# Kernel optimization log

Hardware: AMD Instinct MI355X
Metric: run time of the kernel (lower is better)

Reference implementation:

```python
import jax, jax.numpy as jnp
import numpy as np


def setup_inputs() -> dict:
    key = jax.random.key(0)
    k1, k2, k3, k4 = jax.random.split(key, 4)
    B, D, H, A, T = 1024, 512, 512, 18, 64
    xs = jax.random.normal(k1, (B, D), dtype=jnp.float32)
    task_id = jax.random.randint(k2, (B,), 0, T, dtype=jnp.int64)
    # weight_init ~ scaled randn; biases start at zero per the module
    fc1_weights = jax.random.normal(k3, (T, D, H), dtype=jnp.float32) * (1.0 / np.sqrt(D))
    fc1_biases = jnp.zeros((T, H), dtype=jnp.float32)
    fc2_weights = jax.random.normal(k4, (T, H, A), dtype=jnp.float32) * (1.0 / np.sqrt(H))
    fc2_biases = jnp.zeros((T, A), dtype=jnp.float32)
    return {"xs": xs, "task_id": task_id, "fc1_weights": fc1_weights,
            "fc1_biases": fc1_biases, "fc2_weights": fc2_weights, "fc2_biases": fc2_biases}


def reference(xs, task_id, fc1_weights, fc1_biases, fc2_weights, fc2_biases):
    # per-sample task-indexed weight gather (as in the torch module)
    w1 = fc1_weights[task_id]            # [B, D, H]
    b1 = fc1_biases[task_id]             # [B, H]
    w2 = fc2_weights[task_id]            # [B, H, A]
    b2 = fc2_biases[task_id]             # [B, A]
    h = jax.nn.relu(jnp.einsum('bd,bdh->bh', xs, w1) + b1)   # batch_linear + relu
    logits = jnp.einsum('bh,bha->ba', h, w2) + b2             # batch_linear
    logp = jax.nn.log_softmax(logits, axis=-1)                # [B, A]
    # Categorical sample (fixed key for reproducibility)
    action = jax.random.categorical(jax.random.key(1), logits, axis=-1)  # [B]
    log_prob = jnp.take_along_axis(logp, action[:, None], axis=1)        # [B, 1]
    entropy = -jnp.sum(jnp.exp(logp) * logp, axis=1, keepdims=True)      # [B, 1]
    return action, log_prob, entropy
```

## Files before the change

### kernel.cpp

```cpp
#include <hip/hip_runtime.h>
#include <stdint.h>

#define B_N   1024
#define D_DIM 512
#define H_DIM 512
#define A_DIM 18
#define T_N   64
#define HTILE 256
#define SMAX  32

__device__ __forceinline__ bool taskid_is_int32(const int* raw, int lane) {
    int probe = raw[lane];
    unsigned long long odd = __ballot((lane & 1) && probe != 0);
    return odd != 0ull;
}

template <int KSP>
__global__ __launch_bounds__(256) void fc1_kernel(const float* __restrict__ xs,
                                                  const float* __restrict__ w1,
                                                  const int* __restrict__ raw,
                                                  float* __restrict__ hpre) {
    constexpr int DK = D_DIM / KSP;
    int task  = blockIdx.x;
    int htile = blockIdx.y;
    int ksp   = blockIdx.z;
    int lane = threadIdx.x & 63;
    int wv4  = threadIdx.x >> 6;

    __shared__ int slist[B_N];
    __shared__ int s_n;
    __shared__ __align__(16) float xlds[SMAX * DK];

    if (threadIdx.x < 64) {
        bool is32 = taskid_is_int32(raw, lane);
        int base = 0;
        for (int c = 0; c < B_N; c += 64) {
            int id = is32 ? raw[c + lane] : raw[2 * (c + lane)];
            unsigned long long m = __ballot(id == task);
            if (id == task) {
                unsigned long long below = m & ((1ull << lane) - 1ull);
                slist[base + __popcll(below)] = c + lane;
            }
            base += __popcll(m);
        }
        if (lane == 0) s_n = base;
    }
    __syncthreads();
    int n = s_n;
    if (n == 0) return;

    int hbase = htile * HTILE + lane * 4;
    int d0    = ksp * DK;
    const float* wbase = w1 + ((size_t)task * D_DIM + d0) * H_DIM + hbase;
    float* hout = hpre + (size_t)ksp * ((size_t)B_N * H_DIM);

    for (int sb = 0; sb < n; sb += SMAX) {
        int ns = min(SMAX, n - sb);
        for (int idx = threadIdx.x; idx < ns * DK; idx += 256) {
            int sl = idx / DK;
            int dl = idx - sl * DK;
            int smp = slist[sb + sl];
            xlds[idx] = xs[(size_t)smp * D_DIM + d0 + dl];
        }
        __syncthreads();

        float4 acc[8];
#pragma unroll
        for (int j = 0; j < 8; ++j) acc[j] = make_float4(0.f, 0.f, 0.f, 0.f);

        for (int d = 0; d < DK; d += 8) {
            float4 wvr[8];
#pragma unroll
            for (int u = 0; u < 8; ++u)
                wvr[u] = *(const float4*)(wbase + (size_t)(d + u) * H_DIM);
#pragma unroll
            for (int j = 0; j < 8; ++j) {
                int sl = wv4 + 4 * j;
                if (sl < ns) {
                    const float* xp = &xlds[sl * DK + d];
                    float4 xa = *(const float4*)xp;
                    float4 xb = *(const float4*)(xp + 4);
                    float xv[8] = {xa.x, xa.y, xa.z, xa.w, xb.x, xb.y, xb.z, xb.w};
#pragma unroll
                    for (int u = 0; u < 8; ++u) {
                        acc[j].x = fmaf(xv[u], wvr[u].x, acc[j].x);
                        acc[j].y = fmaf(xv[u], wvr[u].y, acc[j].y);
                        acc[j].z = fmaf(xv[u], wvr[u].z, acc[j].z);
                        acc[j].w = fmaf(xv[u], wvr[u].w, acc[j].w);
                    }
                }
            }
        }

#pragma unroll
        for (int j = 0; j < 8; ++j) {
            int sl = wv4 + 4 * j;
            if (sl < ns) {
                int smp = slist[sb + sl];
                *(float4*)(hout + (size_t)smp * H_DIM + hbase) = acc[j];
            }
        }
        __syncthreads();
    }
}

__device__ __forceinline__ uint32_t rotl32(uint32_t x, int r) {
    return (x << r) | (x >> (32 - r));
}

__device__ __forceinline__ uint32_t threefry_bits_part(uint32_t i) {
    uint32_t x0 = 0u;
    uint32_t x1 = i;
    const uint32_t ks0 = 0u, ks1 = 1u, ks2 = 0x1BD11BDAu ^ 0u ^ 1u;
    x0 += ks0; x1 += ks1;
#define TFR(r) { x0 += x1; x1 = rotl32(x1, (r)); x1 ^= x0; }
    TFR(13) TFR(15) TFR(26) TFR(6)
    x0 += ks1; x1 += ks2 + 1u;
    TFR(17) TFR(29) TFR(16) TFR(24)
    x0 += ks2; x1 += ks0 + 2u;
    TFR(13) TFR(15) TFR(26) TFR(6)
    x0 += ks0; x1 += ks1 + 3u;
    TFR(17) TFR(29) TFR(16) TFR(24)
    x0 += ks1; x1 += ks2 + 4u;
    TFR(13) TFR(15) TFR(26) TFR(6)
    x0 += ks2; x1 += ks0 + 5u;
#undef TFR
    return x0 ^ x1;
}

template <int KSP>
__global__ __launch_bounds__(64) void head_kernel(const int* __restrict__ raw,
                                                  const float* __restrict__ hpre,
                                                  const float* __restrict__ b1,
                                                  const float* __restrict__ w2,
                                                  const float* __restrict__ b2,
                                                  float* __restrict__ out) {
    __shared__ __align__(16) float w2l[H_DIM * A_DIM];
    __shared__ float red[16][A_DIM];
    __shared__ float logits_lds[A_DIM];

    int s = blockIdx.x;
    int lane = threadIdx.x;
    bool is32 = taskid_is_int32(raw, lane);
    int t = is32 ? raw[s] : raw[2 * s];

    const float4* g4 = (const float4*)(w2 + (size_t)t * (H_DIM * A_DIM));
    float4* l4 = (float4*)w2l;
#pragma unroll
    for (int i = 0; i < (H_DIM * A_DIM) / (64 * 4); ++i)
        l4[i * 64 + lane] = g4[i * 64 + lane];

    float hreg[H_DIM / 64];
#pragma unroll
    for (int k = 0; k < H_DIM / 64; ++k) {
        int h = lane + 64 * k;
        size_t p = (size_t)s * H_DIM + h;
        float v = b1[(size_t)t * H_DIM + h];
#pragma unroll
        for (int q = 0; q < KSP; ++q)
            v += hpre[(size_t)q * ((size_t)B_N * H_DIM) + p];
        hreg[k] = fmaxf(v, 0.f);
    }
    __syncthreads();

    float la[A_DIM];
#pragma unroll
    for (int a = 0; a < A_DIM; ++a) la[a] = 0.f;
#pragma unroll
    for (int k = 0; k < H_DIM / 64; ++k) {
        int h = lane + 64 * k;
        const float2* row = (const float2*)&w2l[h * A_DIM];
        float hk = hreg[k];
#pragma unroll
        for (int a2 = 0; a2 < A_DIM / 2; ++a2) {
            float2 ww = row[a2];
            la[2 * a2]     = fmaf(hk, ww.x, la[2 * a2]);
            la[2 * a2 + 1] = fmaf(hk, ww.y, la[2 * a2 + 1]);
        }
    }

#pragma unroll
    for (int a = 0; a < A_DIM; ++a) {
        la[a] += __shfl_xor(la[a], 1);
        la[a] += __shfl_xor(la[a], 2);
    }
    if ((lane & 3) == 0) {
        int g = lane >> 2;
#pragma unroll
        for (int a = 0; a < A_DIM; ++a) red[g][a] = la[a];
    }
    __syncthreads();
    if (lane < A_DIM) {
        float sum = b2[(size_t)t * A_DIM + lane];
#pragma unroll
        for (int g = 0; g < 16; ++g) sum += red[g][lane];
        logits_lds[lane] = sum;
    }
    __syncthreads();

    float lg = (lane < A_DIM) ? logits_lds[lane] : -INFINITY;

    float z = -INFINITY;
    if (lane < A_DIM) {
        uint32_t bits = threefry_bits_part((uint32_t)(s * A_DIM + lane));
        float f = __uint_as_float(0x3f800000u | (bits >> 9)) - 1.0f;
        float u = fmaxf(f, 1.17549435e-38f);
        float g = -logf(-logf(u));
        z = lg + g;
    }
    int idx = lane;
#pragma unroll
    for (int o = 1; o < 64; o <<= 1) {
        float oz = __shfl_xor(z, o);
        int   oi = __shfl_xor(idx, o);
        if (oz > z || (oz == z && oi < idx)) { z = oz; idx = oi; }
    }

    float mx = lg;
#pragma unroll
    for (int o = 1; o < 64; o <<= 1) mx = fmaxf(mx, __shfl_xor(mx, o));
    float e = (lane < A_DIM) ? expf(lg - mx) : 0.f;
#pragma unroll
    for (int o = 1; o < 64; o <<= 1) e += __shfl_xor(e, o);
    float lse = mx + logf(e);
    float lp = lg - lse;
    float c = (lane < A_DIM) ? expf(lp) * lp : 0.f;
#pragma unroll
    for (int o = 1; o < 64; o <<= 1) c += __shfl_xor(c, o);

    if (lane == 0) {
        out[s]             = (float)idx;
        out[B_N + s]       = logits_lds[idx] - lse;
        out[2 * B_N + s]   = -c;
    }
}

extern "C" void kernel_launch(void* const* d_in, const int* in_sizes, int n_in,
                              void* d_out, int out_size, void* d_ws, size_t ws_size,
                              hipStream_t stream) {
    const float* xs      = (const float*)d_in[0];
    const int*   traw    = (const int*)d_in[1];
    const float* w1      = (const float*)d_in[2];
    const float* b1      = (const float*)d_in[3];
    const float* w2      = (const float*)d_in[4];
    const float* b2      = (const float*)d_in[5];
    float* out = (float*)d_out;
    char*  ws  = (char*)d_ws;

    const size_t part_bytes = (size_t)B_N * H_DIM * sizeof(float);

    int ksp = 4;
    if (ws_size < 4 * part_bytes) ksp = 2;
    if (ws_size < 2 * part_bytes) ksp = 1;

    float* hpre = (float*)ws;

    if (ksp == 4) {
        fc1_kernel<4><<<dim3(T_N, 2, 4), 256, 0, stream>>>(xs, w1, traw, hpre);
        head_kernel<4><<<B_N, 64, 0, stream>>>(traw, hpre, b1, w2, b2, out);
    } else if (ksp == 2) {
        fc1_kernel<2><<<dim3(T_N, 2, 2), 256, 0, stream>>>(xs, w1, traw, hpre);
        head_kernel<2><<<B_N, 64, 0, stream>>>(traw, hpre, b1, w2, b2, out);
    } else {
        fc1_kernel<1><<<dim3(T_N, 2, 1), 256, 0, stream>>>(xs, w1, traw, hpre);
        head_kernel<1><<<B_N, 64, 0, stream>>>(traw, hpre, b1, w2, b2, out);
    }
}
```

Baseline: 133.1 us.

## Restructure fc1 to one column per thread with double-buffered weight loads

The fc1 kernel now gives each thread one H column and keeps accumulators for up to 32 samples in registers. Previously each thread covered four columns for a strided subset of samples. Weights are loaded as scalar columns in chunks of 16 rows and double-buffered, so the next chunk's loads overlap the FMAs of the current chunk. Every weight element is now reused across all samples in the thread instead of being reloaded by each of the four waves. The costs are higher register pressure (32 accumulators plus 32 weight registers), a broadcast LDS read pattern for x, and padding samples up to a multiple of 8. The xlds indexing assumes DK/4 == 32, which holds only for KSP=4.

```diff
diff --git a/kernel.cpp b/kernel.cpp
--- a/kernel.cpp
+++ b/kernel.cpp
@@ -21,17 +21,18 @@
                                                   const int* __restrict__ raw,
                                                   float* __restrict__ hpre) {
     constexpr int DK = D_DIM / KSP;
+    constexpr int NCHUNK = DK / 16;
     int task  = blockIdx.x;
     int htile = blockIdx.y;
     int ksp   = blockIdx.z;
-    int lane = threadIdx.x & 63;
-    int wv4  = threadIdx.x >> 6;
+    int tid   = threadIdx.x;
+    int lane  = tid & 63;
 
     __shared__ int slist[B_N];
     __shared__ int s_n;
-    __shared__ __align__(16) float xlds[SMAX * DK];
-
-    if (threadIdx.x < 64) {
+    __shared__ __align__(16) float xlds[SMAX][DK];
+
+    if (tid < 64) {
         bool is32 = taskid_is_int32(raw, lane);
         int base = 0;
         for (int c = 0; c < B_N; c += 64) {
@@ -49,55 +50,81 @@
     int n = s_n;
     if (n == 0) return;
 
-    int hbase = htile * HTILE + lane * 4;
-    int d0    = ksp * DK;
-    const float* wbase = w1 + ((size_t)task * D_DIM + d0) * H_DIM + hbase;
-    float* hout = hpre + (size_t)ksp * ((size_t)B_N * H_DIM);
+    int col = htile * HTILE + tid;
+    int d0  = ksp * DK;
+    const float* wcol = w1 + ((size_t)task * D_DIM + d0) * H_DIM + col;
+    float* hout = hpre + (size_t)ksp * ((size_t)B_N * H_DIM) + col;
 
     for (int sb = 0; sb < n; sb += SMAX) {
-        int ns = min(SMAX, n - sb);
-        for (int idx = threadIdx.x; idx < ns * DK; idx += 256) {
-            int sl = idx / DK;
-            int dl = idx - sl * DK;
-            int smp = slist[sb + sl];
-            xlds[idx] = xs[(size_t)smp * D_DIM + d0 + dl];
-        }
-        __syncthreads();
-
-        float4 acc[8];
-#pragma unroll
-        for (int j = 0; j < 8; ++j) acc[j] = make_float4(0.f, 0.f, 0.f, 0.f);
-
-        for (int d = 0; d < DK; d += 8) {
-            float4 wvr[8];
-#pragma unroll
-            for (int u = 0; u < 8; ++u)
-                wvr[u] = *(const float4*)(wbase + (size_t)(d + u) * H_DIM);
-#pragma unroll
-            for (int j = 0; j < 8; ++j) {
-                int sl = wv4 + 4 * j;
-                if (sl < ns) {
-                    const float* xp = &xlds[sl * DK + d];
-                    float4 xa = *(const float4*)xp;
-                    float4 xb = *(const float4*)(xp + 4);
-                    float xv[8] = {xa.x, xa.y, xa.z, xa.w, xb.x, xb.y, xb.z, xb.w};
-#pragma unroll
-                    for (int u = 0; u < 8; ++u) {
-                        acc[j].x = fmaf(xv[u], wvr[u].x, acc[j].x);
-                        acc[j].y = fmaf(xv[u], wvr[u].y, acc[j].y);
-                        acc[j].z = fmaf(xv[u], wvr[u].z, acc[j].z);
-                        acc[j].w = fmaf(xv[u], wvr[u].w, acc[j].w);
-                    }
-                }
-            }
-        }
-
-#pragma unroll
-        for (int j = 0; j < 8; ++j) {
-            int sl = wv4 + 4 * j;
+        int ns  = min(SMAX, n - sb);
+        int nsr = (ns + 7) & ~7;
+
+        for (int idx = tid; idx < nsr * (DK / 4); idx += 256) {
+            int sl = idx >> 5;
+            int f  = idx & (DK / 4 - 1);
+            float4 v = make_float4(0.f, 0.f, 0.f, 0.f);
             if (sl < ns) {
                 int smp = slist[sb + sl];
-                *(float4*)(hout + (size_t)smp * H_DIM + hbase) = acc[j];
+                v = *(const float4*)(xs + (size_t)smp * D_DIM + d0 + 4 * f);
+            }
+            *(float4*)(&xlds[sl][4 * f]) = v;
+        }
+        __syncthreads();
+
+        float acc[SMAX];
+#pragma unroll
+        for (int j = 0; j < SMAX; ++j) acc[j] = 0.f;
+
+        float wa[16], wb[16];
+
+#define LOADW(buf, cc)                                                        \
+        _Pragma("unroll")                                                     \
+        for (int u = 0; u < 16; ++u)                                          \
+            buf[u] = wcol[(size_t)((cc) * 16 + u) * H_DIM];
+
+#define COMPW(buf, cc) do {                                                   \
+        int dbase = (cc) * 16;                                                \
+        _Pragma("unroll")                                                     \
+        for (int jb = 0; jb < SMAX / 8; ++jb) {                               \
+            if (jb * 8 < nsr) {                                               \
+                _Pragma("unroll")                                             \
+                for (int jj = 0; jj < 8; ++jj) {                              \
+                    int j = jb * 8 + jj;                                      \
+                    float4 x0 = *(const float4*)(&xlds[j][dbase]);            \
+                    float4 x1 = *(const float4*)(&xlds[j][dbase + 4]);        \
+                    float4 x2 = *(const float4*)(&xlds[j][dbase + 8]);        \
+                    float4 x3 = *(const float4*)(&xlds[j][dbase + 12]);       \
+                    float xv[16] = {x0.x, x0.y, x0.z, x0.w,                   \
+                                    x1.x, x1.y, x1.z, x1.w,                   \
+                                    x2.x, x2.y, x2.z, x2.w,                   \
+                                    x3.x, x3.y, x3.z, x3.w};                  \
+                    _Pragma("unroll")                                         \
+                    for (int u = 0; u < 16; ++u)                              \
+                        acc[j] = fmaf(xv[u], buf[u], acc[j]);                 \
+                }                                                             \
+            }                                                                 \
+        }                                                                     \
+    } while (0)
+
+        LOADW(wa, 0);
+#pragma unroll
+        for (int c = 0; c < NCHUNK; ++c) {
+            if ((c & 1) == 0) {
+                if (c + 1 < NCHUNK) { LOADW(wb, c + 1); }
+                COMPW(wa, c);
+            } else {
+                if (c + 1 < NCHUNK) { LOADW(wa, c + 1); }
+                COMPW(wb, c);
+            }
+        }
+#undef LOADW
+#undef COMPW
+
+#pragma unroll
+        for (int j = 0; j < SMAX; ++j) {
+            if (j < ns) {
+                int smp = slist[sb + j];
+                hout[(size_t)smp * H_DIM] = acc[j];
             }
         }
         __syncthreads();
```

Result: slower. 178.1 us (+33.8%).

## Precompute task buckets once and split fc1/head work across sample groups

Applied to the files above, without the earlier changes.

A new single-block bucket kernel counts samples per task, prefix-sums the counts, and writes a sorted sample list to workspace. fc1 blocks no longer each scan all 1024 task ids; the grid is split along samples into NSB groups with smaller 16-sample tiles and double-buffered weight loads. The head kernel now runs per task with w2 staged once into shared memory and reused by four waves over many samples, rather than reloading the 36KB w2 slice for every sample. The cost is an extra kernel launch and repeated w1 reads across the sample-group blocks.

```diff
diff --git a/kernel.cpp b/kernel.cpp
--- a/kernel.cpp
+++ b/kernel.cpp
@@ -7,7 +7,13 @@
 #define A_DIM 18
 #define T_N   64
 #define HTILE 256
-#define SMAX  32
+#define SMB   16
+#define NSB   4
+#define NSB2  8
+
+#define META_OFF   0
+#define META_SLIST 256
+#define META_INTS  2048
 
 __device__ __forceinline__ bool taskid_is_int32(const int* raw, int lane) {
     int probe = raw[lane];
@@ -15,88 +21,133 @@
     return odd != 0ull;
 }
 
+__global__ __launch_bounds__(1024) void bucket_kernel(const int* __restrict__ raw,
+                                                      int* __restrict__ meta) {
+    __shared__ int cnt[T_N];
+    __shared__ int base[T_N];
+    __shared__ int flag32;
+    int tid = threadIdx.x;
+    if (tid < 64) {
+        bool is32 = taskid_is_int32(raw, tid);
+        if (tid == 0) flag32 = is32 ? 1 : 0;
+    }
+    if (tid < T_N) cnt[tid] = 0;
+    __syncthreads();
+    int id = flag32 ? raw[tid] : raw[2 * tid];
+    atomicAdd(&cnt[id], 1);
+    __syncthreads();
+    if (tid < 64) {
+        int v = cnt[tid];
+        int x = v;
+#pragma unroll
+        for (int o = 1; o < 64; o <<= 1) {
+            int tv = __shfl_up(x, o);
+            if (tid >= o) x += tv;
+        }
+        int excl = x - v;
+        meta[META_OFF + tid] = excl;
+        base[tid] = excl;
+        if (tid == 63) meta[META_OFF + 64] = x;
+    }
+    __syncthreads();
+    int pos = atomicAdd(&base[id], 1);
+    meta[META_SLIST + pos] = tid;
+}
+
 template <int KSP>
 __global__ __launch_bounds__(256) void fc1_kernel(const float* __restrict__ xs,
                                                   const float* __restrict__ w1,
-                                                  const int* __restrict__ raw,
+                                                  const int* __restrict__ meta,
                                                   float* __restrict__ hpre) {
     constexpr int DK = D_DIM / KSP;
-    int task  = blockIdx.x;
+    constexpr int NCHUNK = DK / 8;
+    int bx    = blockIdx.x;
+    int task  = bx % T_N;
+    int sb    = bx / T_N;
     int htile = blockIdx.y;
     int ksp   = blockIdx.z;
-    int lane = threadIdx.x & 63;
-    int wv4  = threadIdx.x >> 6;
-
-    __shared__ int slist[B_N];
-    __shared__ int s_n;
-    __shared__ __align__(16) float xlds[SMAX * DK];
-
-    if (threadIdx.x < 64) {
-        bool is32 = taskid_is_int32(raw, lane);
-        int base = 0;
-        for (int c = 0; c < B_N; c += 64) {
-            int id = is32 ? raw[c + lane] : raw[2 * (c + lane)];
-            unsigned long long m = __ballot(id == task);
-            if (id == task) {
-                unsigned long long below = m & ((1ull << lane) - 1ull);
-                slist[base + __popcll(below)] = c + lane;
-            }
-            base += __popcll(m);
-        }
-        if (lane == 0) s_n = base;
-    }
-    __syncthreads();
-    int n = s_n;
-    if (n == 0) return;
+    int tid   = threadIdx.x;
+    int lane  = tid & 63;
+    int wv4   = tid >> 6;
+
+    int off0 = meta[META_OFF + task];
+    int n    = meta[META_OFF + task + 1] - off0;
+    if (sb * SMB >= n) return;
+
+    const int* slist = meta + META_SLIST + off0;
+
+    __shared__ __align__(16) float xlds[SMB][DK];
 
     int hbase = htile * HTILE + lane * 4;
     int d0    = ksp * DK;
     const float* wbase = w1 + ((size_t)task * D_DIM + d0) * H_DIM + hbase;
     float* hout = hpre + (size_t)ksp * ((size_t)B_N * H_DIM);
 
-    for (int sb = 0; sb < n; sb += SMAX) {
-        int ns = min(SMAX, n - sb);
-        for (int idx = threadIdx.x; idx < ns * DK; idx += 256) {
-            int sl = idx / DK;
-            int dl = idx - sl * DK;
-            int smp = slist[sb + sl];
-            xlds[idx] = xs[(size_t)smp * D_DIM + d0 + dl];
-        }
-        __syncthreads();
-
-        float4 acc[8];
-#pragma unroll
-        for (int j = 0; j < 8; ++j) acc[j] = make_float4(0.f, 0.f, 0.f, 0.f);
-
-        for (int d = 0; d < DK; d += 8) {
-            float4 wvr[8];
-#pragma unroll
-            for (int u = 0; u < 8; ++u)
-                wvr[u] = *(const float4*)(wbase + (size_t)(d + u) * H_DIM);
-#pragma unroll
-            for (int j = 0; j < 8; ++j) {
-                int sl = wv4 + 4 * j;
-                if (sl < ns) {
-                    const float* xp = &xlds[sl * DK + d];
-                    float4 xa = *(const float4*)xp;
-                    float4 xb = *(const float4*)(xp + 4);
-                    float xv[8] = {xa.x, xa.y, xa.z, xa.w, xb.x, xb.y, xb.z, xb.w};
-#pragma unroll
-                    for (int u = 0; u < 8; ++u) {
-                        acc[j].x = fmaf(xv[u], wvr[u].x, acc[j].x);
-                        acc[j].y = fmaf(xv[u], wvr[u].y, acc[j].y);
-                        acc[j].z = fmaf(xv[u], wvr[u].z, acc[j].z);
-                        acc[j].w = fmaf(xv[u], wvr[u].w, acc[j].w);
-                    }
-                }
+    for (int sbase = sb * SMB; sbase < n; sbase += NSB * SMB) {
+        int ns = min(SMB, n - sbase);
+
+        for (int idx = tid; idx < SMB * (DK / 4); idx += 256) {
+            int sl = idx / (DK / 4);
+            int f  = idx - sl * (DK / 4);
+            if (sl < ns) {
+                int smp = slist[sbase + sl];
+                *(float4*)(&xlds[sl][4 * f]) =
+                    *(const float4*)(xs + (size_t)smp * D_DIM + d0 + 4 * f);
             }
         }
-
-#pragma unroll
-        for (int j = 0; j < 8; ++j) {
+        __syncthreads();
+
+        float4 acc[SMB / 4];
+#pragma unroll
+        for (int j = 0; j < SMB / 4; ++j) acc[j] = make_float4(0.f, 0.f, 0.f, 0.f);
+
+        float4 wva[8], wvb[8];
+
+#define LOADW(buf, cc)                                                        \
+        _Pragma("unroll")                                                     \
+        for (int u = 0; u < 8; ++u)                                           \
+            buf[u] = *(const float4*)(wbase + (size_t)((cc) * 8 + u) * H_DIM);
+
+#define COMPW(buf, cc) do {                                                   \
+        _Pragma("unroll")                                                     \
+        for (int j = 0; j < SMB / 4; ++j) {                                   \
+            int sl = wv4 + 4 * j;                                             \
+            if (sl < ns) {                        \
+                const float* xp = &xlds[sl][8 * (cc)];                        \
+                float4 xa = *(const float4*)xp;                               \
+                float4 xb = *(const float4*)(xp + 4);                         \
+                float xv[8] = {xa.x, xa.y, xa.z, xa.w,                        \
+                               xb.x, xb.y, xb.z, xb.w};                       \
+                _Pragma("unroll")                                             \
+                for (int u = 0; u < 8; ++u) {                                 \
+                    acc[j].x = fmaf(xv[u], buf[u].x, acc[j].x);               \
+                    acc[j].y = fmaf(xv[u], buf[u].y, acc[j].y);               \
+                    acc[j].z = fmaf(xv[u], buf[u].z, acc[j].z);               \
+                    acc[j].w = fmaf(xv[u], buf[u].w, acc[j].w);               \
+                }                                                             \
+            }                                                                 \
+        }                                                                     \
+    } while (0)
+
+        LOADW(wva, 0);
+#pragma unroll
+        for (int c = 0; c < NCHUNK; ++c) {
+            if ((c & 1) == 0) {
+                if (c + 1 < NCHUNK) { LOADW(wvb, c + 1); }
+                COMPW(wva, c);
+            } else {
+                if (c + 1 < NCHUNK) { LOADW(wva, c + 1); }
+                COMPW(wvb, c);
+            }
+        }
+#undef LOADW
+#undef COMPW
+
+#pragma unroll
+        for (int j = 0; j < SMB / 4; ++j) {
             int sl = wv4 + 4 * j;
             if (sl < ns) {
-                int smp = slist[sb + sl];
+                int smp = slist[sbase + sl];
                 *(float4*)(hout + (size_t)smp * H_DIM + hbase) = acc[j];
             }
         }
@@ -129,109 +180,124 @@
 }
 
 template <int KSP>
-__global__ __launch_bounds__(64) void head_kernel(const int* __restrict__ raw,
-                                                  const float* __restrict__ hpre,
-                                                  const float* __restrict__ b1,
-                                                  const float* __restrict__ w2,
-                                                  const float* __restrict__ b2,
-                                                  float* __restrict__ out) {
+__global__ __launch_bounds__(256) void head_kernel(const int* __restrict__ meta,
+                                                   const float* __restrict__ hpre,
+                                                   const float* __restrict__ b1,
+                                                   const float* __restrict__ w2,
+                                                   const float* __restrict__ b2,
+                                                   float* __restrict__ out) {
     __shared__ __align__(16) float w2l[H_DIM * A_DIM];
-    __shared__ float red[16][A_DIM];
-    __shared__ float logits_lds[A_DIM];
-
-    int s = blockIdx.x;
-    int lane = threadIdx.x;
-    bool is32 = taskid_is_int32(raw, lane);
-    int t = is32 ? raw[s] : raw[2 * s];
+    __shared__ float red[4][16][A_DIM];
+    __shared__ float logits_lds[4][A_DIM];
+
+    int t    = blockIdx.x;
+    int y    = blockIdx.y;
+    int tid  = threadIdx.x;
+    int lane = tid & 63;
+    int wv   = tid >> 6;
+
+    int off0 = meta[META_OFF + t];
+    int n    = meta[META_OFF + t + 1] - off0;
+    if (4 * y >= n) return;
+    int K = (n - 4 * y - 1) / 32 + 1;
+
+    const int* slist = meta + META_SLIST + off0;
 
     const float4* g4 = (const float4*)(w2 + (size_t)t * (H_DIM * A_DIM));
     float4* l4 = (float4*)w2l;
 #pragma unroll
-    for (int i = 0; i < (H_DIM * A_DIM) / (64 * 4); ++i)
-        l4[i * 64 + lane] = g4[i * 64 + lane];
-
-    float hreg[H_DIM / 64];
-#pragma unroll
-    for (int k = 0; k < H_DIM / 64; ++k) {
-        int h = lane + 64 * k;
-        size_t p = (size_t)s * H_DIM + h;
-        float v = b1[(size_t)t * H_DIM + h];
-#pragma unroll
-        for (int q = 0; q < KSP; ++q)
-            v += hpre[(size_t)q * ((size_t)B_N * H_DIM) + p];
-        hreg[k] = fmaxf(v, 0.f);
-    }
+    for (int i = 0; i < (H_DIM * A_DIM) / (256 * 4); ++i)
+        l4[i * 256 + tid] = g4[i * 256 + tid];
     __syncthreads();
 
-    float la[A_DIM];
-#pragma unroll
-    for (int a = 0; a < A_DIM; ++a) la[a] = 0.f;
-#pragma unroll
-    for (int k = 0; k < H_DIM / 64; ++k) {
-        int h = lane + 64 * k;
-        const float2* row = (const float2*)&w2l[h * A_DIM];
-        float hk = hreg[k];
-#pragma unroll
-        for (int a2 = 0; a2 < A_DIM / 2; ++a2) {
-            float2 ww = row[a2];
-            la[2 * a2]     = fmaf(hk, ww.x, la[2 * a2]);
-            la[2 * a2 + 1] = fmaf(hk, ww.y, la[2 * a2 + 1]);
-        }
-    }
-
-#pragma unroll
-    for (int a = 0; a < A_DIM; ++a) {
-        la[a] += __shfl_xor(la[a], 1);
-        la[a] += __shfl_xor(la[a], 2);
-    }
-    if ((lane & 3) == 0) {
-        int g = lane >> 2;
-#pragma unroll
-        for (int a = 0; a < A_DIM; ++a) red[g][a] = la[a];
-    }
-    __syncthreads();
-    if (lane < A_DIM) {
-        float sum = b2[(size_t)t * A_DIM + lane];
-#pragma unroll
-        for (int g = 0; g < 16; ++g) sum += red[g][lane];
-        logits_lds[lane] = sum;
-    }
-    __syncthreads();
-
-    float lg = (lane < A_DIM) ? logits_lds[lane] : -INFINITY;
-
-    float z = -INFINITY;
-    if (lane < A_DIM) {
-        uint32_t bits = threefry_bits_part((uint32_t)(s * A_DIM + lane));
-        float f = __uint_as_float(0x3f800000u | (bits >> 9)) - 1.0f;
-        float u = fmaxf(f, 1.17549435e-38f);
-        float g = -logf(-logf(u));
-        z = lg + g;
-    }
-    int idx = lane;
-#pragma unroll
-    for (int o = 1; o < 64; o <<= 1) {
-        float oz = __shfl_xor(z, o);
-        int   oi = __shfl_xor(idx, o);
-        if (oz > z || (oz == z && oi < idx)) { z = oz; idx = oi; }
-    }
-
-    float mx = lg;
-#pragma unroll
-    for (int o = 1; o < 64; o <<= 1) mx = fmaxf(mx, __shfl_xor(mx, o));
-    float e = (lane < A_DIM) ? expf(lg - mx) : 0.f;
-#pragma unroll
-    for (int o = 1; o < 64; o <<= 1) e += __shfl_xor(e, o);
-    float lse = mx + logf(e);
-    float lp = lg - lse;
-    float c = (lane < A_DIM) ? expf(lp) * lp : 0.f;
-#pragma unroll
-    for (int o = 1; o < 64; o <<= 1) c += __shfl_xor(c, o);
-
-    if (lane == 0) {
-        out[s]             = (float)idx;
-        out[B_N + s]       = logits_lds[idx] - lse;
-        out[2 * B_N + s]   = -c;
+    for (int rnd = 0; rnd < K; ++rnd) {
+        int slot = 4 * y + wv + 32 * rnd;
+        bool active = slot < n;
+        int s = active ? slist[slot] : 0;
+
+        float hreg[H_DIM / 64];
+#pragma unroll
+        for (int kk = 0; kk < H_DIM / 64; ++kk) {
+            int h = lane + 64 * kk;
+            size_t p = (size_t)s * H_DIM + h;
+            float v = b1[(size_t)t * H_DIM + h];
+#pragma unroll
+            for (int q = 0; q < KSP; ++q)
+                v += hpre[(size_t)q * ((size_t)B_N * H_DIM) + p];
+            hreg[kk] = fmaxf(v, 0.f);
+        }
+
+        float la[A_DIM];
+#pragma unroll
+        for (int a = 0; a < A_DIM; ++a) la[a] = 0.f;
+#pragma unroll
+        for (int kk = 0; kk < H_DIM / 64; ++kk) {
+            int h = lane + 64 * kk;
+            const float2* row = (const float2*)&w2l[h * A_DIM];
+            float hk = hreg[kk];
+#pragma unroll
+            for (int a2 = 0; a2 < A_DIM / 2; ++a2) {
+                float2 ww = row[a2];
+                la[2 * a2]     = fmaf(hk, ww.x, la[2 * a2]);
+                la[2 * a2 + 1] = fmaf(hk, ww.y, la[2 * a2 + 1]);
+            }
+        }
+
+#pragma unroll
+        for (int a = 0; a < A_DIM; ++a) {
+            la[a] += __shfl_xor(la[a], 1);
+            la[a] += __shfl_xor(la[a], 2);
+        }
+        if ((lane & 3) == 0) {
+            int g = lane >> 2;
+#pragma unroll
+            for (int a = 0; a < A_DIM; ++a) red[wv][g][a] = la[a];
+        }
+        __syncthreads();
+        if (lane < A_DIM) {
+            float sum = b2[(size_t)t * A_DIM + lane];
+#pragma unroll
+            for (int g = 0; g < 16; ++g) sum += red[wv][g][lane];
+            logits_lds[wv][lane] = sum;
+        }
+        __syncthreads();
+
+        float lg = (lane < A_DIM) ? logits_lds[wv][lane] : -INFINITY;
+
+        float z = -INFINITY;
+        if (lane < A_DIM) {
+            uint32_t bits = threefry_bits_part((uint32_t)(s * A_DIM + lane));
+            float f = __uint_as_float(0x3f800000u | (bits >> 9)) - 1.0f;
+            float u = fmaxf(f, 1.17549435e-38f);
+            float g = -logf(-logf(u));
+            z = lg + g;
+        }
+        int idx = lane;
+#pragma unroll
+        for (int o = 1; o < 64; o <<= 1) {
+            float oz = __shfl_xor(z, o);
+            int   oi = __shfl_xor(idx, o);
+            if (oz > z || (oz == z && oi < idx)) { z = oz; idx = oi; }
+        }
+
+        float mx = lg;
+#pragma unroll
+        for (int o = 1; o < 64; o <<= 1) mx = fmaxf(mx, __shfl_xor(mx, o));
+        float e = (lane < A_DIM) ? expf(lg - mx) : 0.f;
+#pragma unroll
+        for (int o = 1; o < 64; o <<= 1) e += __shfl_xor(e, o);
+        float lse = mx + logf(e);
+        float lp = lg - lse;
+        float c = (lane < A_DIM) ? expf(lp) * lp : 0.f;
+#pragma unroll
+        for (int o = 1; o < 64; o <<= 1) c += __shfl_xor(c, o);
+
+        if (active && lane == 0) {
+            out[s]             = (float)idx;
+            out[B_N + s]       = logits_lds[wv][idx] - lse;
+            out[2 * B_N + s]   = -c;
+        }
+        __syncthreads();
     }
 }
 
@@ -247,22 +313,26 @@
     float* out = (float*)d_out;
     char*  ws  = (char*)d_ws;
 
+    const size_t meta_bytes = META_INTS * sizeof(int);
     const size_t part_bytes = (size_t)B_N * H_DIM * sizeof(float);
 
     int ksp = 4;
-    if (ws_size < 4 * part_bytes) ksp = 2;
-    if (ws_size < 2 * part_bytes) ksp = 1;
-
-    float* hpre = (float*)ws;
+    if (ws_size < meta_bytes + 4 * part_bytes) ksp = 2;
+    if (ws_size < meta_bytes + 2 * part_bytes) ksp = 1;
+
+    int*   meta = (int*)ws;
+    float* hpre = (float*)(ws + meta_bytes);
+
+    bucket_kernel<<<1, 1024, 0, stream>>>(traw, meta);
 
     if (ksp == 4) {
-        fc1_kernel<4><<<dim3(T_N, 2, 4), 256, 0, stream>>>(xs, w1, traw, hpre);
-        head_kernel<4><<<B_N, 64, 0, stream>>>(traw, hpre, b1, w2, b2, out);
+        fc1_kernel<4><<<dim3(T_N * NSB, 2, 4), 256, 0, stream>>>(xs, w1, meta, hpre);
+        head_kernel<4><<<dim3(T_N, NSB2), 256, 0, stream>>>(meta, hpre, b1, w2, b2, out);
     } else if (ksp == 2) {
-        fc1_kernel<2><<<dim3(T_N, 2, 2), 256, 0, stream>>>(xs, w1, traw, hpre);
-        head_kernel<2><<<B_N, 64, 0, stream>>>(traw, hpre, b1, w2, b2, out);
+        fc1_kernel<2><<<dim3(T_N * NSB, 2, 2), 256, 0, stream>>>(xs, w1, meta, hpre);
+        head_kernel<2><<<dim3(T_N, NSB2), 256, 0, stream>>>(meta, hpre, b1, w2, b2, out);
     } else {
-        fc1_kernel<1><<<dim3(T_N, 2, 1), 256, 0, stream>>>(xs, w1, traw, hpre);
-        head_kernel<1><<<B_N, 64, 0, stream>>>(traw, hpre, b1, w2, b2, out);
-    }
-}
+        fc1_kernel<1><<<dim3(T_N * NSB, 2, 1), 256, 0, stream>>>(xs, w1, meta, hpre);
+        head_kernel<1><<<dim3(T_N, NSB2), 256, 0, stream>>>(meta, hpre, b1, w2, b2, out);
+    }
+}
```

After: 206.0 us. 1.55x slower.
